# Kernel tuning notes

Hardware: AMD Instinct MI355X
Metric: run time of the kernel (lower is better)

## Reference

```python
import jax, jax.numpy as jnp
import numpy as np
import math

N_HEADS = 16
ROPE_THETA = 10000.0


def _rope_cos_sin(seqlen, head_dim, theta=ROPE_THETA):
    # freqs_cis = polar(1, outer(t, 1/theta^(2i/d))) -> return cos, sin parts
    inv = 1.0 / (theta ** (jnp.arange(0, head_dim, 2, dtype=jnp.float32) / head_dim))
    t = jnp.arange(seqlen, dtype=jnp.float32)
    freqs = t[:, None] * inv[None, :]          # [S, hd/2]
    return jnp.cos(freqs), jnp.sin(freqs)


def _apply_rope(x, cos, sin):
    # x: [B, S, H, hd]; treat consecutive pairs as complex, rotate by e^{i*freq}
    B, S, H, hd = x.shape
    x2 = x.astype(jnp.float32).reshape(B, S, H, hd // 2, 2)
    xr, xi = x2[..., 0], x2[..., 1]
    c = cos[None, :, None, :]
    s = sin[None, :, None, :]
    out_r = xr * c - xi * s
    out_i = xr * s + xi * c
    return jnp.stack([out_r, out_i], axis=-1).reshape(B, S, H, hd).astype(x.dtype)


def setup_inputs() -> dict:
    key = jax.random.key(0)
    ks = jax.random.split(key, 5)
    dim = 2048
    B, S = 2, 2048
    scale = 1.0 / math.sqrt(dim)
    x = jax.random.normal(ks[0], (B, S, dim), dtype=jnp.float32)
    wq = jax.random.normal(ks[1], (dim, dim), dtype=jnp.float32) * scale
    wk = jax.random.normal(ks[2], (dim, dim), dtype=jnp.float32) * scale
    wv = jax.random.normal(ks[3], (dim, dim), dtype=jnp.float32) * scale
    wo = jax.random.normal(ks[4], (dim, dim), dtype=jnp.float32) * scale
    return {"x": x, "wq": wq, "wk": wk, "wv": wv, "wo": wo}


def reference(x, wq, wk, wv, wo):
    B, S, D = x.shape
    H = N_HEADS
    hd = D // H
    # nn.Linear(bias=False): y = x @ W.T
    q = (x @ wq.T).reshape(B, S, H, hd)
    k = (x @ wk.T).reshape(B, S, H, hd)
    v = (x @ wv.T).reshape(B, S, H, hd)
    cos, sin = _rope_cos_sin(S, hd)
    q = _apply_rope(q, cos, sin)
    k = _apply_rope(k, cos, sin)
    attn = jnp.einsum('bthd,bThd->bhtT', q, k) / jnp.sqrt(jnp.float32(hd))
    attn = jax.nn.softmax(attn, axis=-1)
    out = jnp.einsum('bhtT,bThd->bthd', attn, v).reshape(B, S, D)
    return out @ wo.T
```

## Files before the change

kernel.cpp:

```cpp
#include <hip/hip_runtime.h>
#include <math.h>

typedef unsigned short u16;
typedef __bf16 bf16x8 __attribute__((ext_vector_type(8)));
typedef short s16x4 __attribute__((ext_vector_type(4)));
typedef short s16x8 __attribute__((ext_vector_type(8)));
typedef float f32x4 __attribute__((ext_vector_type(4)));

#define B_ 2
#define S_ 2048
#define D_ 2048
#define H_ 16
#define HD_ 128
#define M_ 4096
#define N3_ 6144

#define AS1(p) ((__attribute__((address_space(1))) void*)(void*)(p))
#define AS3(p) ((__attribute__((address_space(3))) void*)(p))
#define GLD16(g, l) __builtin_amdgcn_global_load_lds(AS1(g), AS3(l), 16, 0, 0)

__device__ __forceinline__ u16 f2bf(float f) {
  unsigned u = __float_as_uint(f);
  return (u16)((u + 0x7FFFu + ((u >> 16) & 1u)) >> 16);
}
__device__ __forceinline__ float bf2f(u16 v) {
  return __uint_as_float(((unsigned)v) << 16);
}

__global__ void cvt5_k(const float* __restrict__ x, const float* __restrict__ wq,
                       const float* __restrict__ wk, const float* __restrict__ wv,
                       const float* __restrict__ wo, u16* __restrict__ xb,
                       u16* __restrict__ wqkvb, u16* __restrict__ wob) {
  int y = blockIdx.y;
  const float* s;
  u16* d;
  int n4;
  if (y == 0) {
    s = x; d = xb; n4 = M_ * D_ / 4;
  } else {
    s = (y == 1) ? wq : (y == 2) ? wk : (y == 3) ? wv : wo;
    d = (y == 4) ? wob : wqkvb + (size_t)(y - 1) * D_ * D_;
    n4 = D_ * D_ / 4;
  }
  int i = blockIdx.x * 256 + threadIdx.x;
  if (i >= n4) return;
  float4 v = ((const float4*)s)[i];
  ushort4 o;
  o.x = f2bf(v.x); o.y = f2bf(v.y); o.z = f2bf(v.z); o.w = f2bf(v.w);
  ((ushort4*)d)[i] = o;
}

__global__ void rope_tab_k(float2* __restrict__ tab) {
  int t = blockIdx.x * 256 + threadIdx.x;
  if (t >= S_ * 64) return;
  int s = t >> 6, i = t & 63;
  double inv = exp2(-(double)i * (13.287712379549449 / 64.0));
  double fr = (double)s * inv;
  double sv, cv;
  sincos(fr, &sv, &cv);
  tab[t] = make_float2((float)cv, (float)sv);
}

template <typename OT>
__global__ __launch_bounds__(512, 2) void gemm256_k(const u16* __restrict__ A,
                                                    const u16* __restrict__ B,
                                                    OT* __restrict__ C,
                                                    int M, int N, int K) {
  __shared__ alignas(16) u16 sm[65536];
  const int tid = threadIdx.x;
  const int wid = tid >> 6, lane = tid & 63;
  const int quad = lane >> 4, l16 = lane & 15;
  const int wr = wid >> 2, wc = wid & 3;

  const int nby = M >> 8, nbx = N >> 8, nwg = nbx * nby;
  int bid = blockIdx.x;
  int wg = (nwg % 8 == 0) ? (bid % 8) * (nwg >> 3) + (bid >> 3) : bid;
  const int m0 = (wg % nby) << 8, n0 = (wg / nby) << 8;

  const int rr = tid >> 3;
  const int sw8 = ((tid & 7) ^ (rr & 7)) * 8;
  const int gb0 = (rr & 31) + ((rr & 32) << 1);
  const u16* pA0_0 = A + (size_t)(m0 + rr) * K + sw8;
  const u16* pA0_1 = A + (size_t)(m0 + 128 + rr) * K + sw8;
  const u16* pA1_0 = A + (size_t)(m0 + 64 + rr) * K + sw8;
  const u16* pA1_1 = A + (size_t)(m0 + 192 + rr) * K + sw8;
  const u16* pB0_0 = B + (size_t)(n0 + gb0) * K + sw8;
  const u16* pB0_1 = B + (size_t)(n0 + 128 + gb0) * K + sw8;
  const u16* pB1_0 = B + (size_t)(n0 + 32 + gb0) * K + sw8;
  const u16* pB1_1 = B + (size_t)(n0 + 160 + gb0) * K + sw8;
  const int dst0 = wid * 64 * 8, dst1 = (512 + wid * 64) * 8;

  const int pj0 = (quad ^ (l16 & 7)) * 8;
  const int pj1 = ((4 + quad) ^ (l16 & 7)) * 8;

  f32x4 acc[8][4] = {};
  const int NT = K >> 6;

  GLD16(pA0_0, sm + dst0);
  GLD16(pA0_1, sm + dst1);
  GLD16(pB0_0, sm + 32768 + dst0);
  GLD16(pB0_1, sm + 32768 + dst1);
  GLD16(pB1_0, sm + 32768 + 8192 + dst0);
  GLD16(pB1_1, sm + 32768 + 8192 + dst1);
  GLD16(pA1_0, sm + 8192 + dst0);
  GLD16(pA1_1, sm + 8192 + dst1);
  asm volatile("s_waitcnt vmcnt(4)" ::: "memory");
  asm volatile("s_barrier" ::: "memory");

  int koff = 0;
#pragma unroll 1
  for (int t = 0; t < NT; ++t) {
    const int aB = (t & 1) * 16384, bB = 32768 + (t & 1) * 16384;
    const int aN = ((t + 1) & 1) * 16384, bN = 32768 + ((t + 1) & 1) * 16384;
    const bool pre = (t + 1 < NT);
    const int kn = koff + 64;
    bf16x8 a_[4][2], b_[4][2];

#pragma unroll
    for (int m = 0; m < 4; ++m) {
      int rb = aB + (wr * 64 + m * 16 + l16) * 64;
      a_[m][0] = *(const bf16x8*)&sm[rb + pj0];
      a_[m][1] = *(const bf16x8*)&sm[rb + pj1];
    }
#pragma unroll
    for (int n = 0; n < 2; ++n) {
      int rb = bB + (wc * 32 + n * 16 + l16) * 64;
      b_[n][0] = *(const bf16x8*)&sm[rb + pj0];
      b_[n][1] = *(const bf16x8*)&sm[rb + pj1];
    }
    if (pre) { GLD16(pA0_0 + kn, sm + aN + dst0); GLD16(pA0_1 + kn, sm + aN + dst1); }
    asm volatile("s_barrier" ::: "memory");
    __builtin_amdgcn_s_setprio(1);
#pragma unroll
    for (int m = 0; m < 4; ++m)
#pragma unroll
      for (int n = 0; n < 2; ++n) {
        acc[m][n] = __builtin_amdgcn_mfma_f32_16x16x32_bf16(a_[m][0], b_[n][0], acc[m][n], 0, 0, 0);
        acc[m][n] = __builtin_amdgcn_mfma_f32_16x16x32_bf16(a_[m][1], b_[n][1], acc[m][n], 0, 0, 0);
      }
    __builtin_amdgcn_s_setprio(0);
    if (pre) asm volatile("s_waitcnt vmcnt(4)" ::: "memory");
    else     asm volatile("s_waitcnt vmcnt(0)" ::: "memory");
    asm volatile("s_barrier" ::: "memory");

#pragma unroll
    for (int n = 0; n < 2; ++n) {
      int rb = bB + (128 + wc * 32 + n * 16 + l16) * 64;
      b_[2 + n][0] = *(const bf16x8*)&sm[rb + pj0];
      b_[2 + n][1] = *(const bf16x8*)&sm[rb + pj1];
    }
    if (pre) { GLD16(pB0_0 + kn, sm + bN + dst0); GLD16(pB0_1 + kn, sm + bN + dst1); }
    asm volatile("s_barrier" ::: "memory");
    __builtin_amdgcn_s_setprio(1);
#pragma unroll
    for (int m = 0; m < 4; ++m)
#pragma unroll
      for (int n = 0; n < 2; ++n) {
        acc[m][2 + n] = __builtin_amdgcn_mfma_f32_16x16x32_bf16(a_[m][0], b_[2 + n][0], acc[m][2 + n], 0, 0, 0);
        acc[m][2 + n] = __builtin_amdgcn_mfma_f32_16x16x32_bf16(a_[m][1], b_[2 + n][1], acc[m][2 + n], 0, 0, 0);
      }
    __builtin_amdgcn_s_setprio(0);
    if (pre) asm volatile("s_waitcnt vmcnt(4)" ::: "memory");
    else     asm volatile("s_waitcnt vmcnt(0)" ::: "memory");
    asm volatile("s_barrier" ::: "memory");

#pragma unroll
    for (int m = 0; m < 4; ++m) {
      int rb = aB + (128 + wr * 64 + m * 16 + l16) * 64;
      a_[m][0] = *(const bf16x8*)&sm[rb + pj0];
      a_[m][1] = *(const bf16x8*)&sm[rb + pj1];
    }
    if (pre) { GLD16(pB1_0 + kn, sm + bN + 8192 + dst0); GLD16(pB1_1 + kn, sm + bN + 8192 + dst1); }
    asm volatile("s_barrier" ::: "memory");
    __builtin_amdgcn_s_setprio(1);
#pragma unroll
    for (int m = 0; m < 4; ++m)
#pragma unroll
      for (int n = 0; n < 2; ++n) {
        acc[4 + m][n] = __builtin_amdgcn_mfma_f32_16x16x32_bf16(a_[m][0], b_[n][0], acc[4 + m][n], 0, 0, 0);
        acc[4 + m][n] = __builtin_amdgcn_mfma_f32_16x16x32_bf16(a_[m][1], b_[n][1], acc[4 + m][n], 0, 0, 0);
      }
    __builtin_amdgcn_s_setprio(0);
    asm volatile("s_barrier" ::: "memory");

    if (pre) { GLD16(pA1_0 + kn, sm + aN + 8192 + dst0); GLD16(pA1_1 + kn, sm + aN + 8192 + dst1); }
    asm volatile("s_barrier" ::: "memory");
    __builtin_amdgcn_s_setprio(1);
#pragma unroll
    for (int m = 0; m < 4; ++m)
#pragma unroll
      for (int n = 0; n < 2; ++n) {
        acc[4 + m][2 + n] = __builtin_amdgcn_mfma_f32_16x16x32_bf16(a_[m][0], b_[2 + n][0], acc[4 + m][2 + n], 0, 0, 0);
        acc[4 + m][2 + n] = __builtin_amdgcn_mfma_f32_16x16x32_bf16(a_[m][1], b_[2 + n][1], acc[4 + m][2 + n], 0, 0, 0);
      }
    __builtin_amdgcn_s_setprio(0);
    asm volatile("s_waitcnt vmcnt(4)" ::: "memory");
    asm volatile("s_barrier" ::: "memory");
    koff = kn;
  }

#pragma unroll
  for (int m = 0; m < 8; ++m) {
#pragma unroll
    for (int n = 0; n < 4; ++n) {
      int col = n0 + wc * 64 + n * 16 + l16;
#pragma unroll
      for (int r = 0; r < 4; ++r) {
        int row = m0 + wr * 128 + m * 16 + quad * 4 + r;
        if constexpr (sizeof(OT) == 4)
          C[(size_t)row * N + col] = acc[m][n][r];
        else
          C[(size_t)row * N + col] = f2bf(acc[m][n][r]);
      }
    }
  }
}

template <typename OT>
__global__ __launch_bounds__(256) void gemm_bt_k(const u16* __restrict__ A,
                                                 const u16* __restrict__ B,
                                                 OT* __restrict__ C,
                                                 int M, int N, int K) {
  __shared__ alignas(16) u16 As[128 * 32];
  __shared__ alignas(16) u16 Bs[128 * 32];
  const int tid = threadIdx.x;
  const int wave = tid >> 6, lane = tid & 63;
  const int quad = lane >> 4, l16 = lane & 15;
  const int m0 = blockIdx.y * 128, n0 = blockIdx.x * 128;
  const int wm = (wave >> 1) * 64, wn = (wave & 1) * 64;
  const u16* Ag = A + (size_t)m0 * K;
  const u16* Bg = B + (size_t)n0 * K;
  f32x4 acc[4][4] = {};
  const int c0 = tid, c1 = tid + 256;
  const int r0 = c0 >> 2, k0b = (c0 & 3) * 8;
  const int r1 = c1 >> 2, k1b = (c1 & 3) * 8;
  u16* la0 = As + (size_t)(wave * 64) * 8;
  u16* la1 = As + (size_t)(256 + wave * 64) * 8;
  u16* lb0 = Bs + (size_t)(wave * 64) * 8;
  u16* lb1 = Bs + (size_t)(256 + wave * 64) * 8;
  for (int kt = 0; kt < K; kt += 32) {
    GLD16(Ag + (size_t)r0 * K + kt + k0b, la0);
    GLD16(Ag + (size_t)r1 * K + kt + k1b, la1);
    GLD16(Bg + (size_t)r0 * K + kt + k0b, lb0);
    GLD16(Bg + (size_t)r1 * K + kt + k1b, lb1);
    __syncthreads();
    bf16x8 af[4], bfr[4];
#pragma unroll
    for (int i = 0; i < 4; ++i)
      af[i] = *(const bf16x8*)&As[(wm + i * 16 + l16) * 32 + quad * 8];
#pragma unroll
    for (int j = 0; j < 4; ++j)
      bfr[j] = *(const bf16x8*)&Bs[(wn + j * 16 + l16) * 32 + quad * 8];
#pragma unroll
    for (int i = 0; i < 4; ++i)
#pragma unroll
      for (int j = 0; j < 4; ++j)
        acc[i][j] = __builtin_amdgcn_mfma_f32_16x16x32_bf16(af[i], bfr[j], acc[i][j], 0, 0, 0);
    __syncthreads();
  }
#pragma unroll
  for (int i = 0; i < 4; ++i) {
#pragma unroll
    for (int j = 0; j < 4; ++j) {
      int n = n0 + wn + j * 16 + l16;
#pragma unroll
      for (int r = 0; r < 4; ++r) {
        int m = m0 + wm + i * 16 + quad * 4 + r;
        if constexpr (sizeof(OT) == 4)
          C[(size_t)m * N + n] = acc[i][j][r];
        else
          C[(size_t)m * N + n] = f2bf(acc[i][j][r]);
      }
    }
  }
}

__global__ void rope_k(const u16* __restrict__ qkv, const float2* __restrict__ tab,
                       u16* __restrict__ Qr, u16* __restrict__ Kr) {
  const float SCLQ = 0.08838834764831845f * 1.4426950408889634f;
  int t = blockIdx.x * 256 + threadIdx.x;
  int m = t >> 10;
  int h = (t >> 6) & 15;
  int i = t & 63;
  int s = m & (S_ - 1);
  int b = m >> 11;
  float2 cs = tab[(s << 6) | i];
  const u16* qp = qkv + (size_t)m * N3_ + h * HD_ + 2 * i;
  ushort2 qv = *(const ushort2*)qp;
  ushort2 kv = *(const ushort2*)(qp + D_);
  float qr = bf2f(qv.x), qi = bf2f(qv.y);
  float kr = bf2f(kv.x), ki = bf2f(kv.y);
  ushort2 qo, ko;
  qo.x = f2bf((qr * cs.x - qi * cs.y) * SCLQ);
  qo.y = f2bf((qr * cs.y + qi * cs.x) * SCLQ);
  ko.x = f2bf(kr * cs.x - ki * cs.y);
  ko.y = f2bf(kr * cs.y + ki * cs.x);
  size_t o = ((size_t)(b * H_ + h) * S_ + s) * HD_ + 2 * i;
  *(ushort2*)(Qr + o) = qo;
  *(ushort2*)(Kr + o) = ko;
}

__global__ __launch_bounds__(256) void vperm_k(const u16* __restrict__ qkv,
                                               u16* __restrict__ Vp) {
  int bh = blockIdx.y;
  int b = bh >> 4, h = bh & 15;
  int t = blockIdx.x * 256 + threadIdx.x;
  int d = t & 127, g = t >> 7;
  const u16* src = qkv + ((size_t)(b * S_ + 4 * g)) * N3_ + 2 * D_ + h * HD_ + d;
  ushort4 o;
  o.x = src[0];
  o.y = src[N3_];
  o.z = src[2 * N3_];
  o.w = src[3 * N3_];
  *(ushort4*)(Vp + (size_t)bh * S_ * HD_ + (size_t)t * 4) = o;
}

#if __has_builtin(__builtin_amdgcn_mfma_f32_16x16x16bf16_1k)
#define HAS_MFMA16 1
#endif

__global__ __launch_bounds__(1024, 4) void flash_k(const u16* __restrict__ Q,
                                                   const u16* __restrict__ Kc,
                                                   const u16* __restrict__ Vp,
                                                   u16* __restrict__ O) {
  __shared__ alignas(16) u16 sm[32768];
  const int tid = threadIdx.x;
  const int wave = tid >> 6, lane = tid & 63;
  const int quad = lane >> 4, l16 = lane & 15;
  const int qt = blockIdx.x, bh = blockIdx.y;
  const int b = bh >> 4, h = bh & 15;
  const u16* vbase_g = Vp + (size_t)bh * S_ * HD_;

#pragma unroll
  for (int i = 0; i < 4; ++i) {
    int c = i * 1024 + tid, row = c >> 4, jl = c & 15;
    int gj = (jl & 8) | ((jl ^ row) & 7);
    GLD16(Q + ((size_t)bh * S_ + qt * 256 + row) * HD_ + gj * 8,
          sm + (size_t)(i * 1024 + wave * 64) * 8);
  }
  __syncthreads();

  bf16x8 qf[4];
  {
    int row = wave * 16 + l16;
#pragma unroll
    for (int dk = 0; dk < 4; ++dk) {
      int c = dk * 4 + quad, pj = (c & 8) | ((c ^ row) & 7);
      qf[dk] = *(const bf16x8*)&sm[row * 128 + pj * 8];
    }
  }
  __syncthreads();

  {
    int c = tid, row = c >> 4, jl = c & 15;
    int gj = (jl & 8) | ((jl ^ row) & 7);
    GLD16(Kc + ((size_t)bh * S_ + row) * HD_ + gj * 8,
          sm + 16384 + (size_t)(wave * 64) * 8);
    GLD16(vbase_g + (size_t)tid * 8,
          sm + 24576 + (size_t)(wave * 64) * 8);
  }
  __syncthreads();

  f32x4 acco[8] = {};
  f32x4 accl = {};
#ifdef HAS_MFMA16
  const s16x4 ones = {(short)0x3F80, (short)0x3F80, (short)0x3F80, (short)0x3F80};
#else
  union { s16x8 s; bf16x8 b; } onesu;
  onesu.s = (s16x8){(short)0x3F80, (short)0x3F80, (short)0x3F80, (short)0x3F80,
                    (short)0x3F80, (short)0x3F80, (short)0x3F80, (short)0x3F80};
#endif

#pragma unroll 1
  for (int kt = 0; kt < 32; ++kt) {
    u16* cb = sm + ((kt & 1) ? 0 : 16384);
    u16* nb = sm + ((kt & 1) ? 16384 : 0);
    if (kt < 31) {
      int c = tid, row = c >> 4, jl = c & 15;
      int gj = (jl & 8) | ((jl ^ row) & 7);
      GLD16(Kc + ((size_t)bh * S_ + (kt + 1) * 64 + row) * HD_ + gj * 8,
            nb + (size_t)(wave * 64) * 8);
      GLD16(vbase_g + (size_t)(kt + 1) * 8192 + (size_t)tid * 8,
            nb + 8192 + (size_t)(wave * 64) * 8);
    }

    f32x4 sc[4] = {};
#pragma unroll
    for (int k4 = 0; k4 < 4; ++k4) {
      int row = k4 * 16 + l16;
#pragma unroll
      for (int dk = 0; dk < 4; ++dk) {
        int c = dk * 4 + quad, pj = (c & 8) | ((c ^ row) & 7);
        bf16x8 kf = *(const bf16x8*)&cb[row * 128 + pj * 8];
        sc[k4] = __builtin_amdgcn_mfma_f32_16x16x32_bf16(kf, qf[dk], sc[k4], 0, 0, 0);
      }
    }

#ifdef HAS_MFMA16
    s16x4 ap[4];
#pragma unroll
    for (int k4 = 0; k4 < 4; ++k4) {
      f32x4 s = sc[k4];
      union { s16x4 s4; __bf16 bb[4]; } pu;
      pu.bb[0] = (__bf16)__builtin_amdgcn_exp2f(s[0]);
      pu.bb[1] = (__bf16)__builtin_amdgcn_exp2f(s[1]);
      pu.bb[2] = (__bf16)__builtin_amdgcn_exp2f(s[2]);
      pu.bb[3] = (__bf16)__builtin_amdgcn_exp2f(s[3]);
      ap[k4] = pu.s4;
    }
#else
    bf16x8 ap[4];
#pragma unroll
    for (int k4 = 0; k4 < 4; ++k4) {
      f32x4 s = sc[k4];
      union { s16x8 s8; bf16x8 b8; __bf16 bb[8]; } pu;
      pu.s8 = (s16x8){0, 0, 0, 0, 0, 0, 0, 0};
      pu.bb[0] = (__bf16)__builtin_amdgcn_exp2f(s[0]);
      pu.bb[1] = (__bf16)__builtin_amdgcn_exp2f(s[1]);
      pu.bb[2] = (__bf16)__builtin_amdgcn_exp2f(s[2]);
      pu.bb[3] = (__bf16)__builtin_amdgcn_exp2f(s[3]);
      ap[k4] = pu.b8;
    }
#endif

#pragma unroll
    for (int ck = 0; ck < 4; ++ck) {
      int vb = 8192 + (ck * 4 + quad) * 512 + l16 * 4;
#pragma unroll
      for (int df = 0; df < 8; ++df) {
        s16x4 bv = *(const s16x4*)&cb[vb + df * 64];
#ifdef HAS_MFMA16
        acco[df] = __builtin_amdgcn_mfma_f32_16x16x16bf16_1k(ap[ck], bv, acco[df], 0, 0, 0);
#else
        union { s16x8 s8; bf16x8 b8; } vbu;
        vbu.s8 = (s16x8){bv[0], bv[1], bv[2], bv[3], 0, 0, 0, 0};
        acco[df] = __builtin_amdgcn_mfma_f32_16x16x32_bf16(ap[ck], vbu.b8, acco[df], 0, 0, 0);
#endif
      }
#ifdef HAS_MFMA16
      accl = __builtin_amdgcn_mfma_f32_16x16x16bf16_1k(ones, ap[ck], accl, 0, 0, 0);
#else
      accl = __builtin_amdgcn_mfma_f32_16x16x32_bf16(onesu.b, ap[ck], accl, 0, 0, 0);
#endif
    }
    __syncthreads();
  }

  {
    float lv = accl[0];
    float linv[4];
#pragma unroll
    for (int r = 0; r < 4; ++r) linv[r] = 1.0f / __shfl(lv, quad * 4 + r);
    int rowb = qt * 256 + wave * 16 + quad * 4;
#pragma unroll
    for (int df = 0; df < 8; ++df) {
      int col = h * HD_ + df * 16 + l16;
#pragma unroll
      for (int r = 0; r < 4; ++r) {
        union { u16 u; __bf16 bb; } ou;
        ou.bb = (__bf16)(acco[df][r] * linv[r]);
        O[((size_t)(b * S_ + rowb + r)) * D_ + col] = ou.u;
      }
    }
  }
}

extern "C" void kernel_launch(void* const* d_in, const int* in_sizes, int n_in,
                              void* d_out, int out_size, void* d_ws, size_t ws_size,
                              hipStream_t stream) {
  const float* x  = (const float*)d_in[0];
  const float* wq = (const float*)d_in[1];
  const float* wk = (const float*)d_in[2];
  const float* wv = (const float*)d_in[3];
  const float* wo = (const float*)d_in[4];

  size_t off = 0;
  char* ws = (char*)d_ws;
  u16* xb    = (u16*)(ws + off); off += (size_t)M_ * D_ * 2;
  u16* wqkvb = (u16*)(ws + off); off += (size_t)3 * D_ * D_ * 2;
  u16* wob   = (u16*)(ws + off); off += (size_t)D_ * D_ * 2;
  u16* qkv   = (u16*)(ws + off); off += (size_t)M_ * N3_ * 2;
  u16* Qr    = (u16*)(ws + off); off += (size_t)M_ * D_ * 2;
  u16* Kr    = (u16*)(ws + off); off += (size_t)M_ * D_ * 2;
  u16* Vp    = (u16*)(ws + off); off += (size_t)M_ * D_ * 2;
  float2* tab = (float2*)(ws + off); off += (size_t)S_ * 64 * sizeof(float2);
  u16* Ob = qkv;
  if (off > ws_size) return;

  cvt5_k<<<dim3(M_ * D_ / 4 / 256, 5), 256, 0, stream>>>(x, wq, wk, wv, wo, xb, wqkvb, wob);
  rope_tab_k<<<(S_ * 64) / 256, 256, 0, stream>>>(tab);
  gemm256_k<u16><<<(M_ / 256) * (N3_ / 256), 512, 0, stream>>>(xb, wqkvb, qkv, M_, N3_, D_);
  rope_k<<<(M_ * H_ * 64) / 256, 256, 0, stream>>>(qkv, tab, Qr, Kr);
  vperm_k<<<dim3(S_ * HD_ / 4 / 256, B_ * H_), 256, 0, stream>>>(qkv, Vp);
  flash_k<<<dim3(S_ / 256, B_ * H_), 1024, 0, stream>>>(Qr, Kr, Vp, Ob);
  gemm_bt_k<float><<<dim3(D_ / 128, M_ / 128), 256, 0, stream>>>(Ob, wob, (float*)d_out, M_, D_, D_);
}
```

Before: 410.1 us.

## Replace output-projection GEMM with double-buffered 128x256 swizzled LDS pipelined kernel

Replaces the simple 128x128, K=32 output-projection GEMM with a 512-thread kernel that uses 128x256 tiles, K=64 steps and XOR-swizzled LDS. Global-to-LDS loads for the next K step are issued while MFMAs run on the current buffers, with split B halves and s_setprio around the MFMA blocks. A grid remap spreads consecutive workgroups across XCDs. The goal is to hide memory latency and cut LDS bank conflicts and barrier stalls in the final GEMM, at the cost of hand-tuned waitcnt and barrier sequencing that is fragile.

```diff
diff --git a/kernel.cpp b/kernel.cpp
--- a/kernel.cpp
+++ b/kernel.cpp
@@ -217,59 +217,118 @@
 }
 
 template <typename OT>
-__global__ __launch_bounds__(256) void gemm_bt_k(const u16* __restrict__ A,
-                                                 const u16* __restrict__ B,
-                                                 OT* __restrict__ C,
-                                                 int M, int N, int K) {
-  __shared__ alignas(16) u16 As[128 * 32];
-  __shared__ alignas(16) u16 Bs[128 * 32];
+__global__ __launch_bounds__(512, 2) void gemmw_k(const u16* __restrict__ A,
+                                                  const u16* __restrict__ B,
+                                                  OT* __restrict__ C,
+                                                  int M, int N, int K) {
+  __shared__ alignas(16) u16 sm[49152];
   const int tid = threadIdx.x;
-  const int wave = tid >> 6, lane = tid & 63;
+  const int wid = tid >> 6, lane = tid & 63;
   const int quad = lane >> 4, l16 = lane & 15;
-  const int m0 = blockIdx.y * 128, n0 = blockIdx.x * 128;
-  const int wm = (wave >> 1) * 64, wn = (wave & 1) * 64;
-  const u16* Ag = A + (size_t)m0 * K;
-  const u16* Bg = B + (size_t)n0 * K;
+  const int wr = wid >> 2, wc = wid & 3;
+
+  const int nbm = M >> 7, nbn = N >> 8, nwg = nbm * nbn;
+  int bid = blockIdx.x;
+  int wg = (nwg % 8 == 0) ? (bid % 8) * (nwg >> 3) + (bid >> 3) : bid;
+  const int m0 = (wg % nbm) << 7, n0 = (wg / nbm) << 8;
+
+  const int rr = tid >> 3;
+  const int sw8 = ((tid & 7) ^ (rr & 7)) * 8;
+  const int gb0 = (rr & 31) + ((rr & 32) << 1);
+  const u16* pA_0 = A + (size_t)(m0 + rr) * K + sw8;
+  const u16* pA_1 = A + (size_t)(m0 + 64 + rr) * K + sw8;
+  const u16* pB0_0 = B + (size_t)(n0 + gb0) * K + sw8;
+  const u16* pB0_1 = B + (size_t)(n0 + 128 + gb0) * K + sw8;
+  const u16* pB1_0 = B + (size_t)(n0 + 32 + gb0) * K + sw8;
+  const u16* pB1_1 = B + (size_t)(n0 + 160 + gb0) * K + sw8;
+  const int dst0 = wid * 512, dst1 = 4096 + wid * 512;
+
+  const int pj0 = (quad ^ (l16 & 7)) * 8;
+  const int pj1 = ((4 + quad) ^ (l16 & 7)) * 8;
+
   f32x4 acc[4][4] = {};
-  const int c0 = tid, c1 = tid + 256;
-  const int r0 = c0 >> 2, k0b = (c0 & 3) * 8;
-  const int r1 = c1 >> 2, k1b = (c1 & 3) * 8;
-  u16* la0 = As + (size_t)(wave * 64) * 8;
-  u16* la1 = As + (size_t)(256 + wave * 64) * 8;
-  u16* lb0 = Bs + (size_t)(wave * 64) * 8;
-  u16* lb1 = Bs + (size_t)(256 + wave * 64) * 8;
-  for (int kt = 0; kt < K; kt += 32) {
-    GLD16(Ag + (size_t)r0 * K + kt + k0b, la0);
-    GLD16(Ag + (size_t)r1 * K + kt + k1b, la1);
-    GLD16(Bg + (size_t)r0 * K + kt + k0b, lb0);
-    GLD16(Bg + (size_t)r1 * K + kt + k1b, lb1);
-    __syncthreads();
-    bf16x8 af[4], bfr[4];
-#pragma unroll
-    for (int i = 0; i < 4; ++i)
-      af[i] = *(const bf16x8*)&As[(wm + i * 16 + l16) * 32 + quad * 8];
-#pragma unroll
-    for (int j = 0; j < 4; ++j)
-      bfr[j] = *(const bf16x8*)&Bs[(wn + j * 16 + l16) * 32 + quad * 8];
-#pragma unroll
-    for (int i = 0; i < 4; ++i)
-#pragma unroll
-      for (int j = 0; j < 4; ++j)
-        acc[i][j] = __builtin_amdgcn_mfma_f32_16x16x32_bf16(af[i], bfr[j], acc[i][j], 0, 0, 0);
-    __syncthreads();
-  }
-#pragma unroll
-  for (int i = 0; i < 4; ++i) {
-#pragma unroll
-    for (int j = 0; j < 4; ++j) {
-      int n = n0 + wn + j * 16 + l16;
+  const int NT = K >> 6;
+
+  GLD16(pA_0, sm + dst0);          GLD16(pA_1, sm + dst1);
+  GLD16(pB0_0, sm + 16384 + dst0); GLD16(pB0_1, sm + 16384 + dst1);
+  GLD16(pB1_0, sm + 24576 + dst0); GLD16(pB1_1, sm + 24576 + dst1);
+  asm volatile("s_waitcnt vmcnt(2)" ::: "memory");
+  asm volatile("s_barrier" ::: "memory");
+
+  int koff = 0;
+#pragma unroll 1
+  for (int t = 0; t < NT; ++t) {
+    const int aB = (t & 1) * 8192, bB = 16384 + (t & 1) * 16384;
+    const int aN = ((t + 1) & 1) * 8192, bN = 16384 + ((t + 1) & 1) * 16384;
+    const bool pre = (t + 1 < NT);
+    const int kn = koff + 64;
+    bf16x8 a_[4][2], b_[4][2];
+
+#pragma unroll
+    for (int m = 0; m < 4; ++m) {
+      int rb = aB + (wr * 64 + m * 16 + l16) * 64;
+      a_[m][0] = *(const bf16x8*)&sm[rb + pj0];
+      a_[m][1] = *(const bf16x8*)&sm[rb + pj1];
+    }
+#pragma unroll
+    for (int n = 0; n < 2; ++n) {
+      int rb = bB + (wc * 32 + n * 16 + l16) * 64;
+      b_[n][0] = *(const bf16x8*)&sm[rb + pj0];
+      b_[n][1] = *(const bf16x8*)&sm[rb + pj1];
+    }
+    if (pre) {
+      GLD16(pA_0 + kn, sm + aN + dst0);  GLD16(pA_1 + kn, sm + aN + dst1);
+      GLD16(pB0_0 + kn, sm + bN + dst0); GLD16(pB0_1 + kn, sm + bN + dst1);
+    }
+    asm volatile("s_barrier" ::: "memory");
+    __builtin_amdgcn_s_setprio(1);
+#pragma unroll
+    for (int m = 0; m < 4; ++m)
+#pragma unroll
+      for (int n = 0; n < 2; ++n) {
+        acc[m][n] = __builtin_amdgcn_mfma_f32_16x16x32_bf16(a_[m][0], b_[n][0], acc[m][n], 0, 0, 0);
+        acc[m][n] = __builtin_amdgcn_mfma_f32_16x16x32_bf16(a_[m][1], b_[n][1], acc[m][n], 0, 0, 0);
+      }
+    __builtin_amdgcn_s_setprio(0);
+    if (pre) asm volatile("s_waitcnt vmcnt(4)" ::: "memory");
+    else     asm volatile("s_waitcnt vmcnt(0)" ::: "memory");
+    asm volatile("s_barrier" ::: "memory");
+
+#pragma unroll
+    for (int n = 0; n < 2; ++n) {
+      int rb = bB + 8192 + (wc * 32 + n * 16 + l16) * 64;
+      b_[2 + n][0] = *(const bf16x8*)&sm[rb + pj0];
+      b_[2 + n][1] = *(const bf16x8*)&sm[rb + pj1];
+    }
+    if (pre) { GLD16(pB1_0 + kn, sm + bN + 8192 + dst0); GLD16(pB1_1 + kn, sm + bN + 8192 + dst1); }
+    asm volatile("s_barrier" ::: "memory");
+    __builtin_amdgcn_s_setprio(1);
+#pragma unroll
+    for (int m = 0; m < 4; ++m)
+#pragma unroll
+      for (int n = 0; n < 2; ++n) {
+        acc[m][2 + n] = __builtin_amdgcn_mfma_f32_16x16x32_bf16(a_[m][0], b_[2 + n][0], acc[m][2 + n], 0, 0, 0);
+        acc[m][2 + n] = __builtin_amdgcn_mfma_f32_16x16x32_bf16(a_[m][1], b_[2 + n][1], acc[m][2 + n], 0, 0, 0);
+      }
+    __builtin_amdgcn_s_setprio(0);
+    if (pre) asm volatile("s_waitcnt vmcnt(2)" ::: "memory");
+    else     asm volatile("s_waitcnt vmcnt(0)" ::: "memory");
+    asm volatile("s_barrier" ::: "memory");
+    koff = kn;
+  }
+
+#pragma unroll
+  for (int m = 0; m < 4; ++m) {
+#pragma unroll
+    for (int n = 0; n < 4; ++n) {
+      int col = n0 + wc * 64 + n * 16 + l16;
 #pragma unroll
       for (int r = 0; r < 4; ++r) {
-        int m = m0 + wm + i * 16 + quad * 4 + r;
+        int row = m0 + wr * 64 + m * 16 + quad * 4 + r;
         if constexpr (sizeof(OT) == 4)
-          C[(size_t)m * N + n] = acc[i][j][r];
+          C[(size_t)row * N + col] = acc[m][n][r];
         else
-          C[(size_t)m * N + n] = f2bf(acc[i][j][r]);
+          C[(size_t)row * N + col] = f2bf(acc[m][n][r]);
       }
     }
   }
@@ -493,5 +552,5 @@
   rope_k<<<(M_ * H_ * 64) / 256, 256, 0, stream>>>(qkv, tab, Qr, Kr);
   vperm_k<<<dim3(S_ * HD_ / 4 / 256, B_ * H_), 256, 0, stream>>>(qkv, Vp);
   flash_k<<<dim3(S_ / 256, B_ * H_), 1024, 0, stream>>>(Qr, Kr, Vp, Ob);
-  gemm_bt_k<float><<<dim3(D_ / 128, M_ / 128), 256, 0, stream>>>(Ob, wob, (float*)d_out, M_, D_, D_);
-}
+  gemmw_k<float><<<(M_ / 128) * (D_ / 256), 512, 0, stream>>>(Ob, wob, (float*)d_out, M_, D_, D_);
+}
```

Result: faster. 392.0 us (-4.4%).
